# Performance work log

Measured on AMD Instinct MI355X. Metric: run time of the kernel, lower is better.

The kernel has to match this reference:

```python
import jax, jax.numpy as jnp
import numpy as np

B, CZ, E, V, H, W = 256, 512, 512, 4096, 16, 16  # batch, z_channels, embed_dim, vocab, latent HxW


def setup_inputs() -> dict:
    key = jax.random.key(0)
    k0, k1, k2, k3 = jax.random.split(key, 4)
    x = jax.random.normal(k0, (B, CZ, H, W), jnp.float32)          # encoder feature map
    pre_w = jax.random.normal(k1, (E, CZ), jnp.float32) * 0.02     # 1x1 pre_quant_conv weight
    pre_b = jnp.zeros((E,), jnp.float32)
    emb = jax.random.uniform(k2, (V, E), jnp.float32, -1.0 / V, 1.0 / V)  # codebook, uniform init as in module
    post_w = jax.random.normal(k3, (CZ, E), jnp.float32) * 0.02    # 1x1 post_quant_conv weight
    post_b = jnp.zeros((CZ,), jnp.float32)
    return dict(x=x, pre_w=pre_w, pre_b=pre_b, emb=emb, post_w=post_w, post_b=post_b)


def reference(x, pre_w, pre_b, emb, post_w, post_b):
    # pre_quant_conv: 1x1 Conv2d(CZ -> E)
    z = jnp.einsum('bchw,ec->behw', x, pre_w) + pre_b[None, :, None, None]
    b, e, h, w = z.shape
    # flatten spatial: (b h w, e)
    zf = z.transpose(0, 2, 3, 1).reshape(-1, e)
    # expanded squared-distance to codebook: ||z||^2 + ||c||^2 - 2 z.c
    dist = (jnp.sum(zf * zf, axis=1, keepdims=True)
            + jnp.sum(emb * emb, axis=1)
            - 2.0 * zf @ emb.T)                                    # [bhw, V]
    tokens = jnp.argmin(dist, axis=-1)                             # [bhw] int
    z_q = emb[tokens].reshape(b, h, w, e).transpose(0, 3, 1, 2)    # gather -> [b,e,h,w]
    # straight-through estimator
    dec_in = z + jax.lax.stop_gradient(z_q - z)
    # post_quant_conv: 1x1 Conv2d(E -> CZ)
    rec = jnp.einsum('behw,ce->bchw', dec_in, post_w) + post_b[None, :, None, None]
    return z, z_q, rec
```

## Files before the change

### kernel.cpp

```cpp
#include <hip/hip_runtime.h>
#include <hip/hip_bf16.h>

typedef unsigned short u16;
typedef unsigned char  u8;
typedef unsigned int   u32;
typedef unsigned long long u64;

using short8 = __attribute__((ext_vector_type(8))) short;
using f32x4  = __attribute__((ext_vector_type(4))) float;
using u16x8  = __attribute__((ext_vector_type(8))) unsigned short;
using ll2    = __attribute__((ext_vector_type(2))) long long;

#define AS_GLOBAL __attribute__((address_space(1)))
#define AS_LDS    __attribute__((address_space(3)))

__device__ __forceinline__ u16 f2b(float x){
  u32 u = __float_as_uint(x);
  u32 r = (u + 0x7FFFu + ((u >> 16) & 1u)) >> 16;
  return (u16)r;
}
__device__ __forceinline__ float b2f(u16 h){ return __uint_as_float(((u32)h) << 16); }

__device__ __forceinline__ u32 f2e4m3(float x){
  float ax = fabsf(x);
  u32 s = (__float_as_uint(x) & 0x80000000u) >> 24;
  ax = fminf(ax, 448.0f);
  if (ax < 0.015625f){
    u32 m = (u32)__float2int_rn(ax * 512.0f);
    return s | m;
  }
  u32 u = __float_as_uint(ax);
  u32 man = u & 0x7FFFFFu;
  u32 rnd = man + 0x7FFFFu + ((man >> 20) & 1u);
  u32 e = (u >> 23) + (rnd >> 23);
  u32 m = (rnd >> 23) ? 0u : ((rnd >> 20) & 7u);
  if (e > 135u) return s | 0x7Eu;
  return s | ((e - 120u) << 3) | m;
}

__device__ __forceinline__ void gload16(u16* l, const u16* g){
  __builtin_amdgcn_global_load_lds((const AS_GLOBAL u32*)g, (AS_LDS u32*)l, 16, 0, 0);
}

__device__ __forceinline__ u64 umin64(u64 a, u64 b){ return a < b ? a : b; }

__device__ __forceinline__ u64 shfl_xor_u64(u64 v, int m){
  u32 lo = __shfl_xor((u32)v, m, 64);
  u32 hi = __shfl_xor((u32)(v >> 32), m, 64);
  return ((u64)hi << 32) | lo;
}

__global__ void k_cvt(const float* __restrict__ w, u16* __restrict__ d, int n){
  int i = blockIdx.x * 256 + threadIdx.x;
  if (i < n) d[i] = f2b(w[i]);
}

__global__ void k_cvt8(const float* __restrict__ src, u8* __restrict__ dst){
  int id = blockIdx.x * 256 + threadIdx.x;
  int row = id >> 7, db = id & 127;
  int b0 = db * 4;
  int kb = b0 >> 6, r6 = b0 & 63;
  int g = r6 >> 4, ks = (r6 >> 3) & 1, j0 = r6 & 7;
  int k = kb * 64 + ks * 32 + g * 8 + j0;
  const float* p = src + (size_t)row * 512 + k;
  u32 w = f2e4m3(p[0] * 1048576.0f)
        | (f2e4m3(p[1] * 1048576.0f) << 8)
        | (f2e4m3(p[2] * 1048576.0f) << 16)
        | (f2e4m3(p[3] * 1048576.0f) << 24);
  *(u32*)(dst + (size_t)row * 512 + b0) = w;
}

__global__ void k_cnorm(const float* __restrict__ emb, float* __restrict__ cn26){
  int v = blockIdx.x, lane = threadIdx.x;
  const float* r = emb + (size_t)v * 512;
  float s = 0.f;
  #pragma unroll
  for (int i = 0; i < 8; ++i){ float x = r[lane + i * 64]; s += x * x; }
  #pragma unroll
  for (int off = 32; off; off >>= 1) s += __shfl_down(s, off, 64);
  if (lane == 0) cn26[v] = s * 67108864.0f;
}

__global__ void k_tcvt(const float* __restrict__ src, u16* __restrict__ d){
  __shared__ float t[64][65];
  const int bid = blockIdx.x;
  const int b  = bid >> 5;
  const int rb = (bid >> 2) & 7;
  const int cb = bid & 3;
  const float* s = src + ((size_t)b * 512 + (size_t)rb * 64) * 256 + cb * 64;
  const int tid = threadIdx.x;
  #pragma unroll
  for (int j = 0; j < 4; ++j){
    int fl = j * 256 + tid;
    int r = fl >> 4, c4 = (fl & 15) * 4;
    float4 v = *(const float4*)(s + (size_t)r * 256 + c4);
    t[r][c4 + 0] = v.x; t[r][c4 + 1] = v.y; t[r][c4 + 2] = v.z; t[r][c4 + 3] = v.w;
  }
  __syncthreads();
  u16* o = d + ((size_t)b * 256 + (size_t)cb * 64) * 512 + rb * 64;
  #pragma unroll
  for (int j = 0; j < 2; ++j){
    int fl = j * 256 + tid;
    int c = fl >> 3, r8 = (fl & 7) * 8;
    u16x8 hv;
    #pragma unroll
    for (int i = 0; i < 8; ++i) hv[i] = f2b(t[r8 + i][c]);
    *(u16x8*)(o + (size_t)c * 512 + r8) = hv;
  }
}

__global__ void k_zq(const u64* __restrict__ keys, const float* __restrict__ emb, float* __restrict__ zq){
  int sidx = blockIdx.x * 64 + threadIdx.x;
  int b = sidx >> 8, s = sidx & 255;
  int v = (int)(u32)keys[sidx];
  const float4* er = (const float4*)(emb + (size_t)v * 512);
  float* o = zq + (size_t)b * 512 * 256 + s;
  #pragma unroll 4
  for (int e4 = 0; e4 < 128; ++e4){
    float4 vv = er[e4];
    o[(size_t)(e4 * 4 + 0) * 256] = vv.x;
    o[(size_t)(e4 * 4 + 1) * 256] = vv.y;
    o[(size_t)(e4 * 4 + 2) * 256] = vv.z;
    o[(size_t)(e4 * 4 + 3) * 256] = vv.w;
  }
}

template<int MODE>
__global__ __launch_bounds__(256, 4) void k_gemm(
    const u16* __restrict__ Ah,
    const u16* __restrict__ Bh,
    const u64* __restrict__ gkeys,
    const float* __restrict__ bias,
    float* __restrict__ Cout,
    u8* __restrict__ Z8,
    int M, int mtbits)
{
  constexpr int K = 512;
  __shared__ __align__(16) u16 sA[128 * 64];
  __shared__ __align__(16) u16 sB[128 * 64];

  const int tid  = threadIdx.x;
  const int lane = tid & 63;
  const int wid  = tid >> 6;
  const int wm = wid >> 1, wn = wid & 1;

  const int nwg = gridDim.x;
  const int chunk = nwg >> 3;
  const int pb = blockIdx.x;
  const int bid = (pb & 7) * chunk + (pb >> 3);

  const int mt = bid & ((1 << mtbits) - 1);
  const int nt = (bid >> mtbits) & 1;
  const int b  = bid >> (mtbits + 1);
  const int m0 = mt * 128;
  const int n0 = nt * 128;
  const int bbase = b * 256;

  const u16* ga[4];
  const u16* gb[4];
  int ldso[4];
  #pragma unroll
  for (int i = 0; i < 4; ++i){
    int e = i * 256 + tid;
    int r = e >> 3;
    int sl = (e & 7) ^ (r & 7);
    ldso[i] = e * 8;
    ga[i] = Ah + (size_t)(m0 + r) * K + sl * 8;
    size_t brow;
    if (MODE == 2) brow = (size_t)(u32)gkeys[bbase + n0 + r];
    else           brow = (size_t)(bbase + n0 + r);
    gb[i] = Bh + brow * K + sl * 8;
  }

  const f32x4 zero4 = {0.f, 0.f, 0.f, 0.f};
  f32x4 acc[4][4];
  #pragma unroll
  for (int i = 0; i < 4; ++i)
    #pragma unroll
    for (int j = 0; j < 4; ++j) acc[i][j] = zero4;

  int aoff[2][4], boff[2][4];
  #pragma unroll
  for (int ks = 0; ks < 2; ++ks)
    #pragma unroll
    for (int f = 0; f < 4; ++f){
      int rA = wm * 64 + f * 16 + (lane & 15);
      aoff[ks][f] = rA * 64 + (((ks * 4 + (lane >> 4)) ^ (rA & 7)) * 8);
      int rB = wn * 64 + f * 16 + (lane & 15);
      boff[ks][f] = rB * 64 + (((ks * 4 + (lane >> 4)) ^ (rB & 7)) * 8);
    }

  for (int kt = 0; kt < 8; ++kt){
    const int k0 = kt * 64;
    #pragma unroll
    for (int i = 0; i < 4; ++i){
      gload16(&sA[ldso[i]], ga[i] + k0);
      gload16(&sB[ldso[i]], gb[i] + k0);
    }
    __syncthreads();
    #pragma unroll
    for (int ks = 0; ks < 2; ++ks){
      short8 ah[4], bh[4];
      #pragma unroll
      for (int f = 0; f < 4; ++f){
        ah[f] = *(const short8*)&sA[aoff[ks][f]];
        bh[f] = *(const short8*)&sB[boff[ks][f]];
      }
      #pragma unroll
      for (int fm = 0; fm < 4; ++fm)
        #pragma unroll
        for (int fn = 0; fn < 4; ++fn)
          acc[fm][fn] = __builtin_amdgcn_mfma_f32_16x16x32_bf16(ah[fm], bh[fn], acc[fm][fn], 0, 0, 0);
    }
    __syncthreads();
  }

  const int row0 = m0 + wm * 64;
  const int col  = n0 + wn * 64 + (lane & 15);
  float* Cb = Cout + (size_t)b * M * 256;
  #pragma unroll
  for (int fm = 0; fm < 4; ++fm){
    #pragma unroll
    for (int j = 0; j < 4; ++j){
      int row = row0 + fm * 16 + (lane >> 4) * 4 + j;
      float bi = bias[row];
      #pragma unroll
      for (int fn = 0; fn < 4; ++fn)
        Cb[(size_t)row * 256 + col + fn * 16] = acc[fm][fn][j] + bi;
    }
  }

  if (MODE == 0){
    #pragma unroll
    for (int fm = 0; fm < 4; ++fm){
      int rb4 = row0 + fm * 16 + (lane >> 4) * 4;
      int pb0 = (rb4 >> 6) * 64 + (((rb4 >> 3) & 3) * 16) + (((rb4 >> 5) & 1) * 8) + (rb4 & 7);
      float bi0 = bias[rb4], bi1 = bias[rb4+1], bi2 = bias[rb4+2], bi3 = bias[rb4+3];
      #pragma unroll
      for (int fn = 0; fn < 4; ++fn){
        u32 w = f2e4m3((acc[fm][fn][0] + bi0) * 64.0f)
              | (f2e4m3((acc[fm][fn][1] + bi1) * 64.0f) << 8)
              | (f2e4m3((acc[fm][fn][2] + bi2) * 64.0f) << 16)
              | (f2e4m3((acc[fm][fn][3] + bi3) * 64.0f) << 24);
        *(u32*)(Z8 + (size_t)(bbase + col + fn * 16) * 512 + pb0) = w;
      }
    }
  }
}

__global__ __launch_bounds__(512, 1) void k_gemm2(
    const u8* __restrict__ A8,
    const u8* __restrict__ B8,
    const float* __restrict__ cn26,
    u64* __restrict__ okeys)
{
  __shared__ __align__(16) u8 lds[163840];

  const int tid  = threadIdx.x;
  const int lane = tid & 63;
  const int wid  = tid >> 6;
  const int wm   = wid >> 2;
  const int wn   = wid & 3;
  const int b    = blockIdx.x;
  const int bbase = b * 256;
  const int g4   = lane >> 4;

#define SB    __builtin_amdgcn_sched_barrier(0)
#define BAR   __builtin_amdgcn_s_barrier()
#define VM2   asm volatile("s_waitcnt vmcnt(2)" ::: "memory")
#define VM0   asm volatile("s_waitcnt vmcnt(0)" ::: "memory")

  #pragma unroll
  for (int i = 0; i < 16; ++i){
    int e = i * 512 + tid;
    int t = e >> 5, s = e & 31;
    gload16((u16*)&lds[e * 16],
            (const u16*)(B8 + (size_t)(bbase + t) * 512 + ((s ^ (t & 31)) * 16)));
  }

  const u8* gsrcA0;
  const u8* gsrcA1;
  {
    int r0 = tid >> 2, s0 = tid & 3;
    int sl0 = (s0 - (r0 >> 1)) & 3;
    gsrcA0 = A8 + (size_t)r0 * 512 + sl0 * 16;
    int r1 = r0 + 128;
    int sl1 = (s0 - (r1 >> 1)) & 3;
    gsrcA1 = A8 + (size_t)r1 * 512 + sl1 * 16;
  }

#define STG_A(tp) { const size_t _o = (size_t)((tp) >> 3) * 131072 + ((tp) & 7) * 64; \
    const int _d = 131072 + (((tp) & 1) * 16384); \
    gload16((u16*)&lds[_d + tid * 16], (const u16*)(gsrcA0 + _o)); \
    gload16((u16*)&lds[_d + 8192 + tid * 16], (const u16*)(gsrcA1 + _o)); }

  int aBase[8];
  #pragma unroll
  for (int fm = 0; fm < 8; ++fm){
    int row = wm * 128 + fm * 16 + (lane & 15);
    int sl = (g4 + ((lane & 15) >> 1)) & 3;
    aBase[fm] = 131072 + row * 64 + sl * 16;
  }
  int tB[4], mB[4];
  #pragma unroll
  for (int fn = 0; fn < 4; ++fn){
    tB[fn] = wn * 64 + fn * 16 + (lane & 15);
    mB[fn] = tB[fn] & 31;
  }

  const f32x4 zero4 = {0.f, 0.f, 0.f, 0.f};
  f32x4 acc[8][4];
  #pragma unroll
  for (int i = 0; i < 8; ++i)
    #pragma unroll
    for (int j = 0; j < 4; ++j) acc[i][j] = zero4;

  u64 best[4];
  #pragma unroll
  for (int i = 0; i < 4; ++i) best[i] = ~0ull;

  STG_A(0)

  for (int mt = 0; mt < 16; ++mt){
    #pragma unroll
    for (int kt = 0; kt < 8; ++kt){
      const int tau = mt * 8 + kt;
      if (tau < 127) STG_A(tau + 1)
      if (tau == 127){ VM0; } else { VM2; }
      SB; BAR; SB;

      const int bufo = (tau & 1) * 16384;
      ll2 af[8], bv[4];
      #pragma unroll
      for (int fm = 0; fm < 8; ++fm)
        af[fm] = *(const ll2*)&lds[aBase[fm] + bufo];
      #pragma unroll
      for (int fn = 0; fn < 4; ++fn)
        bv[fn] = *(const ll2*)&lds[tB[fn] * 512 + (((kt * 4 + g4) ^ mB[fn]) * 16)];

      __builtin_amdgcn_s_setprio(1);
      #pragma unroll
      for (int fm = 0; fm < 8; ++fm)
        #pragma unroll
        for (int fn = 0; fn < 4; ++fn){
          acc[fm][fn] = __builtin_amdgcn_mfma_f32_16x16x32_fp8_fp8(af[fm][0], bv[fn][0], acc[fm][fn], 0, 0, 0);
          acc[fm][fn] = __builtin_amdgcn_mfma_f32_16x16x32_fp8_fp8(af[fm][1], bv[fn][1], acc[fm][fn], 0, 0, 0);
        }
      __builtin_amdgcn_s_setprio(0);
      SB; BAR; SB;
    }

    {
      const float4* cp = (const float4*)(cn26 + mt * 256 + wm * 128 + g4 * 4);
      float4 cnr[8];
      #pragma unroll
      for (int fm = 0; fm < 8; ++fm) cnr[fm] = cp[fm * 4];
      VM0;
      #pragma unroll
      for (int fn = 0; fn < 4; ++fn){
        #pragma unroll
        for (int fm = 0; fm < 8; ++fm){
          #pragma unroll
          for (int jj = 0; jj < 4; ++jj){
            int v = mt * 256 + wm * 128 + fm * 16 + g4 * 4 + jj;
            float sc = ((const float*)&cnr[fm])[jj] - 2.0f * acc[fm][fn][jj];
            u32 o = __float_as_uint(sc);
            o = (o & 0x80000000u) ? ~o : (o | 0x80000000u);
            best[fn] = umin64(best[fn], ((u64)o << 32) | (u32)v);
          }
        }
      }
      #pragma unroll
      for (int i = 0; i < 8; ++i)
        #pragma unroll
        for (int jj = 0; jj < 4; ++jj) acc[i][jj] = zero4;
    }
  }

  #pragma unroll
  for (int fn = 0; fn < 4; ++fn){
    best[fn] = umin64(best[fn], shfl_xor_u64(best[fn], 16));
    best[fn] = umin64(best[fn], shfl_xor_u64(best[fn], 32));
  }
  __syncthreads();
  u64* kbuf = (u64*)&lds[131072];
  if (lane < 16){
    #pragma unroll
    for (int fn = 0; fn < 4; ++fn)
      kbuf[wm * 256 + wn * 64 + fn * 16 + lane] = best[fn];
  }
  __syncthreads();
  if (tid < 256)
    okeys[bbase + tid] = umin64(kbuf[tid], kbuf[256 + tid]);

#undef STG_A
#undef SB
#undef BAR
#undef VM2
#undef VM0
}

extern "C" void kernel_launch(void* const* d_in, const int* in_sizes, int n_in,
                              void* d_out, int out_size, void* d_ws, size_t ws_size,
                              hipStream_t stream){
  const float* x      = (const float*)d_in[0];
  const float* pre_w  = (const float*)d_in[1];
  const float* pre_b  = (const float*)d_in[2];
  const float* emb    = (const float*)d_in[3];
  const float* post_w = (const float*)d_in[4];
  const float* post_b = (const float*)d_in[5];

  float* z_out   = (float*)d_out;
  float* zq_out  = z_out + 33554432;
  float* rec_out = z_out + 67108864;

  char* w = (char*)d_ws;
  u16* prew_b  = (u16*)(w);
  u16* postw_b = (u16*)(w + 524288);
  u16* emb_b   = (u16*)(w + 1048576);
  u8*  emb8    = (u8*)(w + 5242880);
  float* cn26  = (float*)(w + 7340032);
  u64* keys    = (u64*)(w + 7356416);
  u16* xb      = (u16*)(w + 7880704);
  u8*  z8      = (u8*)(w + 74989568);

  k_cvt  <<<1024, 256, 0, stream>>>(pre_w, prew_b, 262144);
  k_cvt  <<<1024, 256, 0, stream>>>(post_w, postw_b, 262144);
  k_cvt  <<<8192, 256, 0, stream>>>(emb, emb_b, 2097152);
  k_cvt8 <<<2048, 256, 0, stream>>>(emb, emb8);
  k_cnorm<<<4096, 64, 0, stream>>>(emb, cn26);

  k_tcvt<<<8192, 256, 0, stream>>>(x, xb);

  k_gemm<0><<<256 * 2 * 4, 256, 0, stream>>>(prew_b, xb,
      nullptr, pre_b, z_out, z8, 512, 2);

  k_gemm2<<<256, 512, 0, stream>>>(emb8, z8, cn26, keys);

  k_zq<<<1024, 64, 0, stream>>>(keys, emb, zq_out);

  k_gemm<2><<<256 * 2 * 4, 256, 0, stream>>>(postw_b, emb_b,
      keys, post_b, rec_out, nullptr, 512, 2);
}
```

Measured before the change: 564.6 us.

## Merge prep kernels into one launch and fuse zq gather with post-conv GEMM

```diff
diff --git a/kernel.cpp b/kernel.cpp
--- a/kernel.cpp
+++ b/kernel.cpp
@@ -50,78 +50,72 @@
   return ((u64)hi << 32) | lo;
 }
 
-__global__ void k_cvt(const float* __restrict__ w, u16* __restrict__ d, int n){
-  int i = blockIdx.x * 256 + threadIdx.x;
-  if (i < n) d[i] = f2b(w[i]);
-}
-
-__global__ void k_cvt8(const float* __restrict__ src, u8* __restrict__ dst){
-  int id = blockIdx.x * 256 + threadIdx.x;
-  int row = id >> 7, db = id & 127;
-  int b0 = db * 4;
-  int kb = b0 >> 6, r6 = b0 & 63;
-  int g = r6 >> 4, ks = (r6 >> 3) & 1, j0 = r6 & 7;
-  int k = kb * 64 + ks * 32 + g * 8 + j0;
-  const float* p = src + (size_t)row * 512 + k;
-  u32 w = f2e4m3(p[0] * 1048576.0f)
-        | (f2e4m3(p[1] * 1048576.0f) << 8)
-        | (f2e4m3(p[2] * 1048576.0f) << 16)
-        | (f2e4m3(p[3] * 1048576.0f) << 24);
-  *(u32*)(dst + (size_t)row * 512 + b0) = w;
-}
-
-__global__ void k_cnorm(const float* __restrict__ emb, float* __restrict__ cn26){
-  int v = blockIdx.x, lane = threadIdx.x;
-  const float* r = emb + (size_t)v * 512;
-  float s = 0.f;
-  #pragma unroll
-  for (int i = 0; i < 8; ++i){ float x = r[lane + i * 64]; s += x * x; }
-  #pragma unroll
-  for (int off = 32; off; off >>= 1) s += __shfl_down(s, off, 64);
-  if (lane == 0) cn26[v] = s * 67108864.0f;
-}
-
-__global__ void k_tcvt(const float* __restrict__ src, u16* __restrict__ d){
+__global__ void k_prep(const float* __restrict__ x,
+                       const float* __restrict__ pre_w,
+                       const float* __restrict__ post_w,
+                       const float* __restrict__ emb,
+                       u16* __restrict__ xb, u16* __restrict__ prew_b,
+                       u16* __restrict__ postw_b, u16* __restrict__ emb_b,
+                       u8* __restrict__ emb8, float* __restrict__ cn26){
   __shared__ float t[64][65];
   const int bid = blockIdx.x;
-  const int b  = bid >> 5;
-  const int rb = (bid >> 2) & 7;
-  const int cb = bid & 3;
-  const float* s = src + ((size_t)b * 512 + (size_t)rb * 64) * 256 + cb * 64;
   const int tid = threadIdx.x;
-  #pragma unroll
-  for (int j = 0; j < 4; ++j){
-    int fl = j * 256 + tid;
-    int r = fl >> 4, c4 = (fl & 15) * 4;
-    float4 v = *(const float4*)(s + (size_t)r * 256 + c4);
-    t[r][c4 + 0] = v.x; t[r][c4 + 1] = v.y; t[r][c4 + 2] = v.z; t[r][c4 + 3] = v.w;
-  }
-  __syncthreads();
-  u16* o = d + ((size_t)b * 256 + (size_t)cb * 64) * 512 + rb * 64;
-  #pragma unroll
-  for (int j = 0; j < 2; ++j){
-    int fl = j * 256 + tid;
-    int c = fl >> 3, r8 = (fl & 7) * 8;
-    u16x8 hv;
-    #pragma unroll
-    for (int i = 0; i < 8; ++i) hv[i] = f2b(t[r8 + i][c]);
-    *(u16x8*)(o + (size_t)c * 512 + r8) = hv;
-  }
-}
-
-__global__ void k_zq(const u64* __restrict__ keys, const float* __restrict__ emb, float* __restrict__ zq){
-  int sidx = blockIdx.x * 64 + threadIdx.x;
-  int b = sidx >> 8, s = sidx & 255;
-  int v = (int)(u32)keys[sidx];
-  const float4* er = (const float4*)(emb + (size_t)v * 512);
-  float* o = zq + (size_t)b * 512 * 256 + s;
-  #pragma unroll 4
-  for (int e4 = 0; e4 < 128; ++e4){
-    float4 vv = er[e4];
-    o[(size_t)(e4 * 4 + 0) * 256] = vv.x;
-    o[(size_t)(e4 * 4 + 1) * 256] = vv.y;
-    o[(size_t)(e4 * 4 + 2) * 256] = vv.z;
-    o[(size_t)(e4 * 4 + 3) * 256] = vv.w;
+
+  if (bid < 8192){
+    const int b  = bid >> 5;
+    const int rb = (bid >> 2) & 7;
+    const int cb = bid & 3;
+    const float* s = x + ((size_t)b * 512 + (size_t)rb * 64) * 256 + cb * 64;
+    #pragma unroll
+    for (int j = 0; j < 4; ++j){
+      int fl = j * 256 + tid;
+      int r = fl >> 4, c4 = (fl & 15) * 4;
+      float4 v = *(const float4*)(s + (size_t)r * 256 + c4);
+      t[r][c4 + 0] = v.x; t[r][c4 + 1] = v.y; t[r][c4 + 2] = v.z; t[r][c4 + 3] = v.w;
+    }
+    __syncthreads();
+    u16* o = xb + ((size_t)b * 256 + (size_t)cb * 64) * 512 + rb * 64;
+    #pragma unroll
+    for (int j = 0; j < 2; ++j){
+      int fl = j * 256 + tid;
+      int c = fl >> 3, r8 = (fl & 7) * 8;
+      u16x8 hv;
+      #pragma unroll
+      for (int i = 0; i < 8; ++i) hv[i] = f2b(t[r8 + i][c]);
+      *(u16x8*)(o + (size_t)c * 512 + r8) = hv;
+    }
+  } else if (bid < 9216){
+    int i = (bid - 8192) * 256 + tid;
+    prew_b[i] = f2b(pre_w[i]);
+  } else if (bid < 10240){
+    int i = (bid - 9216) * 256 + tid;
+    postw_b[i] = f2b(post_w[i]);
+  } else if (bid < 18432){
+    int i = (bid - 10240) * 256 + tid;
+    emb_b[i] = f2b(emb[i]);
+  } else if (bid < 20480){
+    int id = (bid - 18432) * 256 + tid;
+    int row = id >> 7, db = id & 127;
+    int b0 = db * 4;
+    int kb = b0 >> 6, r6 = b0 & 63;
+    int g = r6 >> 4, ks = (r6 >> 3) & 1, j0 = r6 & 7;
+    int k = kb * 64 + ks * 32 + g * 8 + j0;
+    const float* p = emb + (size_t)row * 512 + k;
+    u32 w = f2e4m3(p[0] * 1048576.0f)
+          | (f2e4m3(p[1] * 1048576.0f) << 8)
+          | (f2e4m3(p[2] * 1048576.0f) << 16)
+          | (f2e4m3(p[3] * 1048576.0f) << 24);
+    *(u32*)(emb8 + (size_t)row * 512 + b0) = w;
+  } else {
+    int wv = tid >> 6, lane = tid & 63;
+    int v = (bid - 20480) * 4 + wv;
+    const float* r = emb + (size_t)v * 512;
+    float s = 0.f;
+    #pragma unroll
+    for (int i = 0; i < 8; ++i){ float xx = r[lane + i * 64]; s += xx * xx; }
+    #pragma unroll
+    for (int off = 32; off; off >>= 1) s += __shfl_down(s, off, 64);
+    if (lane == 0) cn26[v] = s * 67108864.0f;
   }
 }
 
@@ -342,10 +336,13 @@
       #pragma unroll
       for (int fm = 0; fm < 8; ++fm)
         #pragma unroll
-        for (int fn = 0; fn < 4; ++fn){
+        for (int fn = 0; fn < 4; ++fn)
           acc[fm][fn] = __builtin_amdgcn_mfma_f32_16x16x32_fp8_fp8(af[fm][0], bv[fn][0], acc[fm][fn], 0, 0, 0);
+      #pragma unroll
+      for (int fm = 0; fm < 8; ++fm)
+        #pragma unroll
+        for (int fn = 0; fn < 4; ++fn)
           acc[fm][fn] = __builtin_amdgcn_mfma_f32_16x16x32_fp8_fp8(af[fm][1], bv[fn][1], acc[fm][fn], 0, 0, 0);
-        }
       __builtin_amdgcn_s_setprio(0);
       SB; BAR; SB;
     }
@@ -400,6 +397,126 @@
 #undef VM0
 }
 
+__global__ __launch_bounds__(256, 4) void k_tail(
+    const u16* __restrict__ Ah,
+    const u16* __restrict__ Bh,
+    const u64* __restrict__ gkeys,
+    const float* __restrict__ bias,
+    float* __restrict__ Cout,
+    const float* __restrict__ emb,
+    float* __restrict__ zq)
+{
+  constexpr int K = 512;
+  __shared__ __align__(16) u16 sA[128 * 64];
+  __shared__ __align__(16) u16 sB[128 * 64];
+
+  const int tid = threadIdx.x;
+
+  if (blockIdx.x >= 2048){
+    int sidx = (blockIdx.x - 2048) * 256 + tid;
+    int b = sidx >> 8, s = sidx & 255;
+    int v = (int)(u32)gkeys[sidx];
+    const float4* er = (const float4*)(emb + (size_t)v * 512);
+    float* o = zq + (size_t)b * 512 * 256 + s;
+    #pragma unroll 4
+    for (int e4 = 0; e4 < 128; ++e4){
+      float4 vv = er[e4];
+      o[(size_t)(e4 * 4 + 0) * 256] = vv.x;
+      o[(size_t)(e4 * 4 + 1) * 256] = vv.y;
+      o[(size_t)(e4 * 4 + 2) * 256] = vv.z;
+      o[(size_t)(e4 * 4 + 3) * 256] = vv.w;
+    }
+    return;
+  }
+
+  const int lane = tid & 63;
+  const int wid  = tid >> 6;
+  const int wm = wid >> 1, wn = wid & 1;
+
+  const int chunk = 2048 >> 3;
+  const int pb = blockIdx.x;
+  const int bid = (pb & 7) * chunk + (pb >> 3);
+
+  const int mt = bid & 3;
+  const int nt = (bid >> 2) & 1;
+  const int b  = bid >> 3;
+  const int m0 = mt * 128;
+  const int n0 = nt * 128;
+  const int bbase = b * 256;
+
+  const u16* ga[4];
+  const u16* gb[4];
+  int ldso[4];
+  #pragma unroll
+  for (int i = 0; i < 4; ++i){
+    int e = i * 256 + tid;
+    int r = e >> 3;
+    int sl = (e & 7) ^ (r & 7);
+    ldso[i] = e * 8;
+    ga[i] = Ah + (size_t)(m0 + r) * K + sl * 8;
+    size_t brow = (size_t)(u32)gkeys[bbase + n0 + r];
+    gb[i] = Bh + brow * K + sl * 8;
+  }
+
+  const f32x4 zero4 = {0.f, 0.f, 0.f, 0.f};
+  f32x4 acc[4][4];
+  #pragma unroll
+  for (int i = 0; i < 4; ++i)
+    #pragma unroll
+    for (int j = 0; j < 4; ++j) acc[i][j] = zero4;
+
+  int aoff[2][4], boff[2][4];
+  #pragma unroll
+  for (int ks = 0; ks < 2; ++ks)
+    #pragma unroll
+    for (int f = 0; f < 4; ++f){
+      int rA = wm * 64 + f * 16 + (lane & 15);
+      aoff[ks][f] = rA * 64 + (((ks * 4 + (lane >> 4)) ^ (rA & 7)) * 8);
+      int rB = wn * 64 + f * 16 + (lane & 15);
+      boff[ks][f] = rB * 64 + (((ks * 4 + (lane >> 4)) ^ (rB & 7)) * 8);
+    }
+
+  for (int kt = 0; kt < 8; ++kt){
+    const int k0 = kt * 64;
+    #pragma unroll
+    for (int i = 0; i < 4; ++i){
+      gload16(&sA[ldso[i]], ga[i] + k0);
+      gload16(&sB[ldso[i]], gb[i] + k0);
+    }
+    __syncthreads();
+    #pragma unroll
+    for (int ks = 0; ks < 2; ++ks){
+      short8 ah[4], bh[4];
+      #pragma unroll
+      for (int f = 0; f < 4; ++f){
+        ah[f] = *(const short8*)&sA[aoff[ks][f]];
+        bh[f] = *(const short8*)&sB[boff[ks][f]];
+      }
+      #pragma unroll
+      for (int fm = 0; fm < 4; ++fm)
+        #pragma unroll
+        for (int fn = 0; fn < 4; ++fn)
+          acc[fm][fn] = __builtin_amdgcn_mfma_f32_16x16x32_bf16(ah[fm], bh[fn], acc[fm][fn], 0, 0, 0);
+    }
+    __syncthreads();
+  }
+
+  const int row0 = m0 + wm * 64;
+  const int col  = n0 + wn * 64 + (lane & 15);
+  float* Cb = Cout + (size_t)b * K * 256;
+  #pragma unroll
+  for (int fm = 0; fm < 4; ++fm){
+    #pragma unroll
+    for (int j = 0; j < 4; ++j){
+      int row = row0 + fm * 16 + (lane >> 4) * 4 + j;
+      float bi = bias[row];
+      #pragma unroll
+      for (int fn = 0; fn < 4; ++fn)
+        Cb[(size_t)row * 256 + col + fn * 16] = acc[fm][fn][j] + bi;
+    }
+  }
+}
+
 extern "C" void kernel_launch(void* const* d_in, const int* in_sizes, int n_in,
                               void* d_out, int out_size, void* d_ws, size_t ws_size,
                               hipStream_t stream){
@@ -424,21 +541,14 @@
   u16* xb      = (u16*)(w + 7880704);
   u8*  z8      = (u8*)(w + 74989568);
 
-  k_cvt  <<<1024, 256, 0, stream>>>(pre_w, prew_b, 262144);
-  k_cvt  <<<1024, 256, 0, stream>>>(post_w, postw_b, 262144);
-  k_cvt  <<<8192, 256, 0, stream>>>(emb, emb_b, 2097152);
-  k_cvt8 <<<2048, 256, 0, stream>>>(emb, emb8);
-  k_cnorm<<<4096, 64, 0, stream>>>(emb, cn26);
-
-  k_tcvt<<<8192, 256, 0, stream>>>(x, xb);
+  k_prep<<<21504, 256, 0, stream>>>(x, pre_w, post_w, emb,
+                                    xb, prew_b, postw_b, emb_b, emb8, cn26);
 
   k_gemm<0><<<256 * 2 * 4, 256, 0, stream>>>(prew_b, xb,
       nullptr, pre_b, z_out, z8, 512, 2);
 
   k_gemm2<<<256, 512, 0, stream>>>(emb8, z8, cn26, keys);
 
-  k_zq<<<1024, 64, 0, stream>>>(keys, emb, zq_out);
-
-  k_gemm<2><<<256 * 2 * 4, 256, 0, stream>>>(postw_b, emb_b,
-      keys, post_b, rec_out, nullptr, 512, 2);
-}
+  k_tail<<<2048 + 256, 256, 0, stream>>>(postw_b, emb_b, keys, post_b,
+                                         rec_out, emb, zq_out);
+}
```

After: 576.3 us. 2.1% more time.
